# Performance work log

Measured on AMD Instinct MI355X. Metric: run time of the kernel, lower is better.

The kernel has to match this reference:

```python
import jax, jax.numpy as jnp
import numpy as np

B = 4096
IN = 1723 * 6          # 10338
H = 1024
OUT = 24 * 3 * 3 + 10 + 3  # 229
EPS = 1e-5


def _bn(x, g, b):
    # BatchNorm1d training-mode forward: biased batch statistics
    mu = jnp.mean(x, axis=0)
    var = jnp.var(x, axis=0)
    return g * (x - mu) * jax.lax.rsqrt(var + EPS) + b


def _resblock(h, wa, ba, ga, bea, wb, bb, gb, beb):
    t = jax.nn.relu(_bn(h @ wa + ba, ga, bea))
    t = _bn(t @ wb + bb, gb, beb)
    return jax.nn.relu(h + t)


def setup_inputs() -> dict:
    key = jax.random.key(0)
    ks = jax.random.split(key, 16)
    s = 0.02
    inp = {"x": jax.random.normal(ks[0], (B, IN), dtype=jnp.float32)}
    # FCBlock(IN -> H): Linear + BN + ReLU
    inp["w1"] = jax.random.normal(ks[1], (IN, H), dtype=jnp.float32) * s
    inp["b1"] = jnp.zeros((H,), jnp.float32)
    inp["g1"] = jnp.ones((H,), jnp.float32)
    inp["be1"] = jnp.zeros((H,), jnp.float32)
    # two FCResBlocks (H -> H)
    for i, kk in zip((2, 3), (ks[2:4], ks[4:6])):
        inp[f"w{i}a"] = jax.random.normal(kk[0], (H, H), dtype=jnp.float32) * s
        inp[f"b{i}a"] = jnp.zeros((H,), jnp.float32)
        inp[f"g{i}a"] = jnp.ones((H,), jnp.float32)
        inp[f"be{i}a"] = jnp.zeros((H,), jnp.float32)
        inp[f"w{i}b"] = jax.random.normal(kk[1], (H, H), dtype=jnp.float32) * s
        inp[f"b{i}b"] = jnp.zeros((H,), jnp.float32)
        inp[f"g{i}b"] = jnp.ones((H,), jnp.float32)
        inp[f"be{i}b"] = jnp.zeros((H,), jnp.float32)
    # final Linear (H -> OUT)
    inp["w4"] = jax.random.normal(ks[6], (H, OUT), dtype=jnp.float32) * s
    inp["b4"] = jnp.zeros((OUT,), jnp.float32)
    return inp


def reference(x, w1, b1, g1, be1,
              w2a, b2a, g2a, be2a, w2b, b2b, g2b, be2b,
              w3a, b3a, g3a, be3a, w3b, b3b, g3b, be3b,
              w4, b4):
    batch = x.shape[0]
    h = jax.nn.relu(_bn(x @ w1 + b1, g1, be1))
    h = _resblock(h, w2a, b2a, g2a, be2a, w2b, b2b, g2b, be2b)
    h = _resblock(h, w3a, b3a, g3a, be3a, w3b, b3b, g3b, be3b)
    out = h @ w4 + b4                              # (B, 229)

    rotmat = out[:, :216].reshape(-1, 3, 3)        # (B*24, 3, 3)
    betas = out[:, 216:226]                        # (B, 10)
    camera = out[:, 226:]                          # (B, 3)

    # batched 3x3 SVD orthogonalization (replaces per-sample Python loop)
    U, S, Vh = jnp.linalg.svd(rotmat, full_matrices=False)
    R = U @ Vh
    # det computed under no_grad in original -> stop_gradient
    det = jax.lax.stop_gradient(jnp.linalg.det(R))[:, None, None]
    R = (R * det).reshape(batch, 24, 3, 3)
    return (R, betas, camera)
```

## Files before the change

### kernel.cpp

```cpp
#include <hip/hip_runtime.h>
#include <math.h>


typedef _Float16 half8 __attribute__((ext_vector_type(8)));
typedef _Float16 half4_t __attribute__((ext_vector_type(4)));
typedef float floatx4 __attribute__((ext_vector_type(4)));

#define LO_SCALE 4096.0f
#define LO_INV (1.0f / 4096.0f)
#define IN_C 10338
#define INP_C 10368

__device__ __forceinline__ void gld16(const _Float16* g, _Float16* l) {
  __builtin_amdgcn_global_load_lds(
      (const __attribute__((address_space(1))) void*)g,
      (__attribute__((address_space(3))) void*)l, 16, 0, 0);
}

template <int TAG, bool STATS>
__global__ __launch_bounds__(256, 2)
void gemm_sk(const _Float16* __restrict__ Ah, const _Float16* __restrict__ Al,
             const _Float16* __restrict__ Bh, const _Float16* __restrict__ Bl,
             float* __restrict__ Cp, int Kld, int Ncols, int Ks,
             size_t partStride, const float* __restrict__ bias,
             float* __restrict__ psum, float* __restrict__ psq) {
  __shared__ _Float16 sAh[2][4096], sAl[2][4096];
  __shared__ _Float16 sBh[2][4096], sBl[2][4096];
  const int tid = threadIdx.x;
  const int wv = tid >> 6, ln = tid & 63;
  const int ln15 = ln & 15, q = ln >> 4;
  const int wr = wv >> 1, wc = wv & 1;
  const int bm0 = blockIdx.x * 128, bn0 = blockIdx.y * 128;
  const int k0 = blockIdx.z * Ks;
  Cp += (size_t)blockIdx.z * partStride;

  const int srow = ln >> 2;
  const int swzw = (ln & 3) ^ (srow & 3) ^ ((srow >> 2) & 3);
  const int ch0 = wv * 2, ch1 = wv * 2 + 1;
  const size_t offA0 = (size_t)(bm0 + ch0 * 16 + srow) * Kld + k0 + swzw * 8;
  const size_t offA1 = (size_t)(bm0 + ch1 * 16 + srow) * Kld + k0 + swzw * 8;
  const size_t offB0 = (size_t)(bn0 + ch0 * 16 + srow) * Kld + k0 + swzw * 8;
  const size_t offB1 = (size_t)(bn0 + ch1 * 16 + srow) * Kld + k0 + swzw * 8;

  const int swzr = (q ^ (ln15 & 3) ^ ((ln15 >> 2) & 3)) * 8;
  const int aoff = (wr * 64 + ln15) * 32 + swzr;
  const int boff = (wc * 64 + ln15) * 32 + swzr;

  floatx4 acc[4][4];
  floatx4 acc2[4][4];
#pragma unroll
  for (int i = 0; i < 4; ++i)
#pragma unroll
    for (int j = 0; j < 4; ++j) {
      acc[i][j] = (floatx4){0.f, 0.f, 0.f, 0.f};
      acc2[i][j] = (floatx4){0.f, 0.f, 0.f, 0.f};
    }

  auto stage = [&](int kt, int buf) {
    gld16(Ah + offA0 + kt, &sAh[buf][ch0 * 512]);
    gld16(Ah + offA1 + kt, &sAh[buf][ch1 * 512]);
    gld16(Al + offA0 + kt, &sAl[buf][ch0 * 512]);
    gld16(Al + offA1 + kt, &sAl[buf][ch1 * 512]);
    gld16(Bh + offB0 + kt, &sBh[buf][ch0 * 512]);
    gld16(Bh + offB1 + kt, &sBh[buf][ch1 * 512]);
    gld16(Bl + offB0 + kt, &sBl[buf][ch0 * 512]);
    gld16(Bl + offB1 + kt, &sBl[buf][ch1 * 512]);
  };

  stage(0, 0);
  int cur = 0;
  for (int kt = 0; kt < Ks; kt += 32) {
    __syncthreads();
    if (kt + 32 < Ks) stage(kt + 32, cur ^ 1);

    const _Float16* pAh = &sAh[cur][aoff];
    const _Float16* pAl = &sAl[cur][aoff];
    const _Float16* pBh = &sBh[cur][boff];
    const _Float16* pBl = &sBl[cur][boff];
    half8 bh[4], bl[4];
#pragma unroll
    for (int ni = 0; ni < 4; ++ni) {
      bh[ni] = *(const half8*)(pBh + ni * 512);
      bl[ni] = *(const half8*)(pBl + ni * 512);
    }
#pragma unroll
    for (int mh = 0; mh < 2; ++mh) {
      half8 ah[2], al[2];
#pragma unroll
      for (int i = 0; i < 2; ++i) {
        ah[i] = *(const half8*)(pAh + (mh * 2 + i) * 512);
        al[i] = *(const half8*)(pAl + (mh * 2 + i) * 512);
      }
#pragma unroll
      for (int i = 0; i < 2; ++i) {
        const int mi = mh * 2 + i;
#pragma unroll
        for (int ni = 0; ni < 4; ++ni) {
          acc[mi][ni] = __builtin_amdgcn_mfma_f32_16x16x32_f16(
              ah[i], bh[ni], acc[mi][ni], 0, 0, 0);
          acc2[mi][ni] = __builtin_amdgcn_mfma_f32_16x16x32_f16(
              ah[i], bl[ni], acc2[mi][ni], 0, 0, 0);
          acc2[mi][ni] = __builtin_amdgcn_mfma_f32_16x16x32_f16(
              al[i], bh[ni], acc2[mi][ni], 0, 0, 0);
        }
      }
    }
    cur ^= 1;
  }

  float bs[4];
  float sacc[4] = {0.f, 0.f, 0.f, 0.f};
  float qacc[4] = {0.f, 0.f, 0.f, 0.f};
  if constexpr (STATS) {
#pragma unroll
    for (int ni = 0; ni < 4; ++ni)
      bs[ni] = bias[bn0 + wc * 64 + ni * 16 + ln15];
  }
#pragma unroll
  for (int mi = 0; mi < 4; ++mi)
#pragma unroll
    for (int ni = 0; ni < 4; ++ni) {
      const int col = bn0 + wc * 64 + ni * 16 + ln15;
      const int rbase = bm0 + wr * 64 + mi * 16 + q * 4;
#pragma unroll
      for (int r = 0; r < 4; ++r) {
        float v = acc[mi][ni][r] + acc2[mi][ni][r] * LO_INV;
        if constexpr (STATS) {
          v += bs[ni];
          sacc[ni] += v;
          qacc[ni] += v * v;
        }
        Cp[(size_t)(rbase + r) * Ncols + col] = v;
      }
    }
  if constexpr (STATS) {
    __syncthreads();
    float* sS = (float*)&sAh[0][0];
    float* sQ = (float*)&sAl[0][0];
    const int contrib = wr * 4 + q;
#pragma unroll
    for (int ni = 0; ni < 4; ++ni) {
      const int colt = wc * 64 + ni * 16 + ln15;
      sS[contrib * 128 + colt] = sacc[ni];
      sQ[contrib * 128 + colt] = qacc[ni];
    }
    __syncthreads();
    if (tid < 128) {
      float S = 0.f, Q = 0.f;
#pragma unroll
      for (int c = 0; c < 8; ++c) {
        S += sS[c * 128 + tid];
        Q += sQ[c * 128 + tid];
      }
      psum[(size_t)blockIdx.x * 1024 + bn0 + tid] = S;
      psq[(size_t)blockIdx.x * 1024 + bn0 + tid] = Q;
    }
  }
}

struct TJob {
  const float* src;
  _Float16* th;
  _Float16* tl;
  int K, N, Kpad, tK, start;
};
struct CJobs {
  TJob j[6];
  const float* x;
  _Float16* xh;
  _Float16* xl;
  int splitStart;
};

__global__ __launch_bounds__(256)
void convert_all(CJobs J) {
  const int b = blockIdx.x;
  const int tid = threadIdx.x;
  if (b >= J.splitStart) {
    int di = (b - J.splitStart) * 256 + tid;
    int base = di * 8;
    int row = base / INP_C;
    int col0 = base - row * INP_C;
    const float* src = J.x + (size_t)row * IN_C + col0;
    float v[8];
#pragma unroll
    for (int j = 0; j < 8; ++j) v[j] = (col0 + j < IN_C) ? src[j] : 0.f;
    half8 h, l;
#pragma unroll
    for (int j = 0; j < 8; ++j) {
      _Float16 hh = (_Float16)v[j];
      h[j] = hh;
      l[j] = (_Float16)((v[j] - (float)hh) * LO_SCALE);
    }
    *(half8*)(J.xh + base) = h;
    *(half8*)(J.xl + base) = l;
    return;
  }
  int ji = 0;
#pragma unroll
  for (int i = 1; i < 6; ++i)
    if (b >= J.j[i].start) ji = i;
  const TJob job = J.j[ji];
  const int t = b - job.start;
  const int kk0 = (t % job.tK) * 32;
  const int nn0 = (t / job.tK) * 32;

  __shared__ float ts[32][33];
  const int tx = tid & 31, ty = tid >> 5;
#pragma unroll
  for (int r = 0; r < 4; ++r) {
    int kk = kk0 + ty + r * 8;
    int nn = nn0 + tx;
    ts[ty + r * 8][tx] =
        (kk < job.K && nn < job.N) ? job.src[(size_t)kk * job.N + nn] : 0.f;
  }
  __syncthreads();
  const int tw = tid & 7, rw = tid >> 3;
  const int nn = nn0 + rw, kk = kk0 + tw * 4;
  half4_t h, l;
#pragma unroll
  for (int i2 = 0; i2 < 4; ++i2) {
    float v = ts[tw * 4 + i2][rw];
    _Float16 hh = (_Float16)v;
    h[i2] = hh;
    l[i2] = (_Float16)((v - (float)hh) * LO_SCALE);
  }
  size_t o = (size_t)nn * job.Kpad + kk;
  *(half4_t*)(job.th + o) = h;
  *(half4_t*)(job.tl + o) = l;
}

__global__ __launch_bounds__(256)
void reduce_bias_stats_v(const float* __restrict__ Cp,
                         const float* __restrict__ bias, float* __restrict__ Y,
                         float* __restrict__ psum, float* __restrict__ psq,
                         int S, size_t stride, int rowsPer) {
  const int N = 1024;
  const int t = threadIdx.x;
  const int cg = t & 15, rl = t >> 4;
  const int col4 = blockIdx.x * 64 + cg * 4;
  const int r0 = blockIdx.y * rowsPer;
  const floatx4 bs = *(const floatx4*)(bias + col4);
  floatx4 s = {0.f, 0.f, 0.f, 0.f}, qq = {0.f, 0.f, 0.f, 0.f};
  for (int r = r0 + rl; r < r0 + rowsPer; r += 16) {
    size_t i = (size_t)r * N + col4;
    floatx4 v = bs;
    for (int k = 0; k < S; ++k) v += *(const floatx4*)(Cp + k * stride + i);
    *(floatx4*)(Y + i) = v;
    s += v;
    qq += v * v;
  }
  __shared__ floatx4 ls[16][16], lq[16][16];
  ls[rl][cg] = s;
  lq[rl][cg] = qq;
  __syncthreads();
  if (t < 16) {
    floatx4 S4 = {0.f, 0.f, 0.f, 0.f}, Q4 = {0.f, 0.f, 0.f, 0.f};
#pragma unroll
    for (int r = 0; r < 16; ++r) {
      S4 += ls[r][t];
      Q4 += lq[r][t];
    }
    size_t o = (size_t)blockIdx.y * N + blockIdx.x * 64 + t * 4;
    *(floatx4*)(psum + o) = S4;
    *(floatx4*)(psq + o) = Q4;
  }
}

__global__ __launch_bounds__(256)
void bn_apply_v(const float* __restrict__ Y, const float* __restrict__ psum,
                const float* __restrict__ psq, const float* __restrict__ g,
                const float* __restrict__ be, const float* __restrict__ res,
                float* __restrict__ outf, _Float16* __restrict__ oh,
                _Float16* __restrict__ ol, int RB, float invM) {
  const int N = 1024;
  const int t = threadIdx.x;
  const int cg = t & 63, rl = t >> 6;
  const int col4 = blockIdx.x * 256 + cg * 4;
  __shared__ floatx4 lA[64], lB[64];
  if (t < 64) {
    int c4 = blockIdx.x * 256 + t * 4;
    floatx4 s = {0.f, 0.f, 0.f, 0.f}, qq = {0.f, 0.f, 0.f, 0.f};
    for (int rb = 0; rb < RB; ++rb) {
      s += *(const floatx4*)(psum + (size_t)rb * N + c4);
      qq += *(const floatx4*)(psq + (size_t)rb * N + c4);
    }
    floatx4 m = s * invM;
    floatx4 var = qq * invM - m * m;
    floatx4 rstd;
#pragma unroll
    for (int i = 0; i < 4; ++i) rstd[i] = rsqrtf(var[i] + 1e-5f);
    floatx4 a = (*(const floatx4*)(g + c4)) * rstd;
    lA[t] = a;
    lB[t] = (*(const floatx4*)(be + c4)) - m * a;
  }
  __syncthreads();
  const floatx4 a = lA[cg], b2 = lB[cg];
#pragma unroll
  for (int rr = 0; rr < 2; ++rr) {
    const int r = blockIdx.y * 8 + rl + rr * 4;
    const size_t i = (size_t)r * N + col4;
    floatx4 v = (*(const floatx4*)(Y + i)) * a + b2;
    if (res) v += *(const floatx4*)(res + i);
#pragma unroll
    for (int ii = 0; ii < 4; ++ii) v[ii] = fmaxf(v[ii], 0.f);
    if (outf) *(floatx4*)(outf + i) = v;
    half4_t h, l;
#pragma unroll
    for (int ii = 0; ii < 4; ++ii) {
      _Float16 hh = (_Float16)v[ii];
      h[ii] = hh;
      l[ii] = (_Float16)((v[ii] - (float)hh) * LO_SCALE);
    }
    *(half4_t*)(oh + i) = h;
    *(half4_t*)(ol + i) = l;
  }
}

__device__ __forceinline__ void cofactor3(const float X[9], float C[9]) {
  C[0] = X[4] * X[8] - X[5] * X[7];
  C[1] = X[5] * X[6] - X[3] * X[8];
  C[2] = X[3] * X[7] - X[4] * X[6];
  C[3] = X[2] * X[7] - X[1] * X[8];
  C[4] = X[0] * X[8] - X[2] * X[6];
  C[5] = X[1] * X[6] - X[0] * X[7];
  C[6] = X[1] * X[5] - X[2] * X[4];
  C[7] = X[2] * X[3] - X[0] * X[5];
  C[8] = X[0] * X[4] - X[1] * X[3];
}

__global__ __launch_bounds__(256)
void polar_tail(const float* __restrict__ Cp, const float* __restrict__ bias,
                float* __restrict__ out, int Bt, int nmat, int S,
                size_t stride) {
  const int ldy = 256;
  int idx = blockIdx.x * blockDim.x + threadIdx.x;
  if (idx < nmat) {
    int s = idx / 24, j = idx % 24;
    const size_t base = (size_t)s * ldy + j * 9;
    float A[9], X[9];
#pragma unroll
    for (int k = 0; k < 9; ++k) {
      float v = bias[j * 9 + k];
      for (int z = 0; z < S; ++z) v += Cp[z * stride + base + k];
      A[k] = v;
      X[k] = v;
    }
    double detA = (double)A[0] * ((double)A[4] * A[8] - (double)A[5] * A[7]) -
                  (double)A[1] * ((double)A[3] * A[8] - (double)A[5] * A[6]) +
                  (double)A[2] * ((double)A[3] * A[7] - (double)A[4] * A[6]);
    float sgn = (detA < 0.0) ? -1.f : 1.f;
#pragma unroll 1
    for (int it = 0; it < 12; ++it) {
      float C[9];
      cofactor3(X, C);
      float det = X[0] * C[0] + X[1] * C[1] + X[2] * C[2];
      float ad = fmaxf(fabsf(det), 1e-30f);
      float idet = (det < 0.f ? -1.f : 1.f) / ad;
      float n1 = 0.f, n2 = 0.f;
#pragma unroll
      for (int k = 0; k < 9; ++k) {
        n1 += X[k] * X[k];
        n2 += C[k] * C[k];
      }
      n1 = fmaxf(n1, 1e-30f);
      float zeta = sqrtf(sqrtf(n2 * idet * idet / n1));
      zeta = fminf(fmaxf(zeta, 1e-4f), 1e4f);
      float iz = 0.5f / zeta;
      float hz = 0.5f * zeta;
#pragma unroll
      for (int k = 0; k < 9; ++k) X[k] = hz * X[k] + iz * idet * C[k];
    }
    float* o = out + (size_t)idx * 9;
#pragma unroll
    for (int k = 0; k < 9; ++k) o[k] = X[k] * sgn;
  } else {
    int i = idx - nmat;
    int nb = Bt * 10;
    int nc = Bt * 3;
    int s, k, c;
    if (i < nb) {
      s = i / 10;
      k = i;
      c = 216 + (i % 10);
    } else if (i < nb + nc) {
      int t2 = i - nb;
      s = t2 / 3;
      k = i;
      c = 226 + (t2 % 3);
    } else {
      return;
    }
    float v = bias[c];
    size_t base = (size_t)s * ldy + c;
    for (int z = 0; z < S; ++z) v += Cp[z * stride + base];
    out[(size_t)Bt * 216 + k] = v;
  }
}

extern "C" void kernel_launch(void* const* d_in, const int* in_sizes, int n_in,
                              void* d_out, int out_size, void* d_ws,
                              size_t ws_size, hipStream_t stream) {
  const float* x = (const float*)d_in[0];
  const float* w1 = (const float*)d_in[1];
  const float* b1 = (const float*)d_in[2];
  const float* g1 = (const float*)d_in[3];
  const float* be1 = (const float*)d_in[4];
  const float* w2a = (const float*)d_in[5];
  const float* b2a = (const float*)d_in[6];
  const float* g2a = (const float*)d_in[7];
  const float* be2a = (const float*)d_in[8];
  const float* w2b = (const float*)d_in[9];
  const float* b2b = (const float*)d_in[10];
  const float* g2b = (const float*)d_in[11];
  const float* be2b = (const float*)d_in[12];
  const float* w3a = (const float*)d_in[13];
  const float* b3a = (const float*)d_in[14];
  const float* g3a = (const float*)d_in[15];
  const float* be3a = (const float*)d_in[16];
  const float* w3b = (const float*)d_in[17];
  const float* b3b = (const float*)d_in[18];
  const float* g3b = (const float*)d_in[19];
  const float* be3b = (const float*)d_in[20];
  const float* w4 = (const float*)d_in[21];
  const float* b4 = (const float*)d_in[22];
  float* out = (float*)d_out;

  const int B = 4096, IN = 10338, INP = 10368, H = 1024;
  const int OUTN = 229, OUTP = 256;
  const int RB = 32;
  const int S_BIG = 2, S_HEAD = 8;

  char* p = (char*)d_ws;
  auto alloc = [&](size_t bytes) -> void* {
    void* r = (void*)p;
    p += (bytes + 255) & ~(size_t)255;
    return r;
  };
  float* Cpart = (float*)alloc((size_t)S_HEAD * B * OUTP * 4);
  float* Y = (float*)alloc((size_t)B * H * 4);
  float* Hf = (float*)alloc((size_t)B * H * 4);
  _Float16* xh = (_Float16*)alloc((size_t)B * INP * 2);
  _Float16* xl = (_Float16*)alloc((size_t)B * INP * 2);
  _Float16* w1h = (_Float16*)alloc((size_t)H * INP * 2);
  _Float16* w1l = (_Float16*)alloc((size_t)H * INP * 2);
  _Float16 *wmh[4], *wml[4];
  for (int i = 0; i < 4; ++i) {
    wmh[i] = (_Float16*)alloc((size_t)H * H * 2);
    wml[i] = (_Float16*)alloc((size_t)H * H * 2);
  }
  _Float16* w4h = (_Float16*)alloc((size_t)OUTP * H * 2);
  _Float16* w4l = (_Float16*)alloc((size_t)OUTP * H * 2);
  _Float16* hh = (_Float16*)alloc((size_t)B * H * 2);
  _Float16* hl = (_Float16*)alloc((size_t)B * H * 2);
  float* psum = (float*)alloc((size_t)RB * H * 4);
  float* psq = (float*)alloc((size_t)RB * H * 4);

  {
    CJobs J;
    const float* wsrc[6] = {w1, w2a, w2b, w3a, w3b, w4};
    _Float16* th[6] = {w1h, wmh[0], wmh[1], wmh[2], wmh[3], w4h};
    _Float16* tl[6] = {w1l, wml[0], wml[1], wml[2], wml[3], w4l};
    int Ks[6] = {IN, H, H, H, H, H};
    int Ns[6] = {H, H, H, H, H, OUTN};
    int Kpads[6] = {INP, H, H, H, H, H};
    int Npads[6] = {H, H, H, H, H, OUTP};
    int start = 0;
    for (int i = 0; i < 6; ++i) {
      J.j[i].src = wsrc[i];
      J.j[i].th = th[i];
      J.j[i].tl = tl[i];
      J.j[i].K = Ks[i];
      J.j[i].N = Ns[i];
      J.j[i].Kpad = Kpads[i];
      J.j[i].tK = Kpads[i] / 32;
      J.j[i].start = start;
      start += (Kpads[i] / 32) * (Npads[i] / 32);
    }
    J.x = x;
    J.xh = xh;
    J.xl = xl;
    J.splitStart = start;
    int total = start + (B * INP / 8 + 255) / 256;
    convert_all<<<dim3(total), 256, 0, stream>>>(J);
  }

  auto bnapply = [&](const float* g, const float* be, const float* res,
                     float* outf) {
    bn_apply_v<<<dim3(H / 256, B / 8), 256, 0, stream>>>(
        Y, psum, psq, g, be, res, outf, hh, hl, RB, 1.f / B);
  };
  auto midgemm = [&](const _Float16* Bh, const _Float16* Bl,
                     const float* bias) {
    gemm_sk<1, true><<<dim3(B / 128, H / 128, 1), 256, 0, stream>>>(
        hh, hl, Bh, Bl, Y, H, H, H, 0, bias, psum, psq);
  };

  gemm_sk<0, false><<<dim3(B / 128, H / 128, S_BIG), 256, 0, stream>>>(
      xh, xl, w1h, w1l, Cpart, INP, H, INP / S_BIG, (size_t)B * H, nullptr,
      nullptr, nullptr);
  reduce_bias_stats_v<<<dim3(16, RB), 256, 0, stream>>>(
      Cpart, b1, Y, psum, psq, S_BIG, (size_t)B * H, B / RB);
  bnapply(g1, be1, nullptr, Hf);
  midgemm(wmh[0], wml[0], b2a);
  bnapply(g2a, be2a, nullptr, nullptr);
  midgemm(wmh[1], wml[1], b2b);
  bnapply(g2b, be2b, Hf, Hf);
  midgemm(wmh[2], wml[2], b3a);
  bnapply(g3a, be3a, nullptr, nullptr);
  midgemm(wmh[3], wml[3], b3b);
  bnapply(g3b, be3b, Hf, Hf);
  gemm_sk<2, false><<<dim3(B / 128, OUTP / 128, S_HEAD), 256, 0, stream>>>(
      hh, hl, w4h, w4l, Cpart, H, OUTP, H / S_HEAD, (size_t)B * OUTP, nullptr,
      nullptr, nullptr);

  int nmat = B * 24;
  int ntot = nmat + B * 13;
  polar_tail<<<dim3((ntot + 255) / 256), 256, 0, stream>>>(
      Cpart, b4, out, B, nmat, S_HEAD, (size_t)B * OUTP);
}
```

Before: 918.9 us.

## Add 256x256-tile 512-thread GEMM for first layer with split-K of four

Adds a dedicated first-layer GEMM kernel that uses 256x256 output tiles per 512-thread block, double-buffered LDS loads and a remapped block index. Split-K goes from 2 to 4, so the grid is one block per CU. The goal is more operand reuse per byte loaded on the dominant K=10368 GEMM. To make room for four partial buffers without more workspace, Y and Hf now alias partitions of the split-K buffer, so restrict qualifiers are dropped from the reduce kernel. The cost is heavy LDS use (one block per CU), more partial-sum traffic in the reduce, and reliance on the reduce reading each element before it overwrites it in place.

```diff
diff --git a/kernel.cpp b/kernel.cpp
--- a/kernel.cpp
+++ b/kernel.cpp
@@ -15,6 +15,125 @@
   __builtin_amdgcn_global_load_lds(
       (const __attribute__((address_space(1))) void*)g,
       (__attribute__((address_space(3))) void*)l, 16, 0, 0);
+}
+
+__global__ __launch_bounds__(512, 2)
+void gemm_l1(const _Float16* __restrict__ Ah, const _Float16* __restrict__ Al,
+             const _Float16* __restrict__ Bh, const _Float16* __restrict__ Bl,
+             float* __restrict__ Cp, int Kld, int Ncols, int Ks,
+             size_t partStride) {
+  __shared__ _Float16 sAh[2][8192], sAl[2][8192];
+  __shared__ _Float16 sBh[2][8192], sBl[2][8192];
+  const int tid = threadIdx.x;
+  const int wv = tid >> 6, ln = tid & 63;
+  const int ln15 = ln & 15, q = ln >> 4;
+  const int wr = wv >> 2, wc = wv & 3;
+  const int xm = (blockIdx.x & 7) * 2 + (blockIdx.x >> 3);
+  const int bm0 = xm * 256, bn0 = blockIdx.y * 256;
+  const int k0 = blockIdx.z * Ks;
+  Cp += (size_t)blockIdx.z * partStride;
+
+  const int srow = ln >> 2;
+  const int swzw = (ln & 3) ^ (srow & 3) ^ ((srow >> 2) & 3);
+  const int ch0 = wv, ch1 = wv + 8;
+  const size_t offA0 = (size_t)(bm0 + ch0 * 16 + srow) * Kld + k0 + swzw * 8;
+  const size_t offA1 = (size_t)(bm0 + ch1 * 16 + srow) * Kld + k0 + swzw * 8;
+  const size_t offB0 = (size_t)(bn0 + ch0 * 16 + srow) * Kld + k0 + swzw * 8;
+  const size_t offB1 = (size_t)(bn0 + ch1 * 16 + srow) * Kld + k0 + swzw * 8;
+
+  const int swzr = (q ^ (ln15 & 3) ^ ((ln15 >> 2) & 3)) * 8;
+
+  floatx4 acc[8][4], acc2[8][4];
+#pragma unroll
+  for (int i = 0; i < 8; ++i)
+#pragma unroll
+    for (int j = 0; j < 4; ++j) {
+      acc[i][j] = (floatx4){0.f, 0.f, 0.f, 0.f};
+      acc2[i][j] = (floatx4){0.f, 0.f, 0.f, 0.f};
+    }
+
+  auto stage = [&](int kt, int buf) {
+    gld16(Bh + offB0 + kt, &sBh[buf][ch0 * 512]);
+    gld16(Bh + offB1 + kt, &sBh[buf][ch1 * 512]);
+    gld16(Bl + offB0 + kt, &sBl[buf][ch0 * 512]);
+    gld16(Bl + offB1 + kt, &sBl[buf][ch1 * 512]);
+    gld16(Ah + offA0 + kt, &sAh[buf][ch0 * 512]);
+    gld16(Ah + offA1 + kt, &sAh[buf][ch1 * 512]);
+    gld16(Al + offA0 + kt, &sAl[buf][ch0 * 512]);
+    gld16(Al + offA1 + kt, &sAl[buf][ch1 * 512]);
+  };
+
+  stage(0, 0);
+  int cur = 0;
+  for (int kt = 0; kt < Ks; kt += 32) {
+    asm volatile("s_waitcnt lgkmcnt(0)" ::: "memory");
+    __builtin_amdgcn_s_barrier();
+    __builtin_amdgcn_sched_barrier(0);
+    if (kt + 32 < Ks) {
+      stage(kt + 32, cur ^ 1);
+      asm volatile("s_waitcnt vmcnt(8)" ::: "memory");
+    } else {
+      asm volatile("s_waitcnt vmcnt(0)" ::: "memory");
+    }
+    __builtin_amdgcn_s_barrier();
+    __builtin_amdgcn_sched_barrier(0);
+
+    const _Float16* pAh = &sAh[cur][0];
+    const _Float16* pAl = &sAl[cur][0];
+    const _Float16* pBh = &sBh[cur][0];
+    const _Float16* pBl = &sBl[cur][0];
+    half8 bhf[4], blf[4];
+#pragma unroll
+    for (int ni = 0; ni < 4; ++ni) {
+      const int bo = (wc * 64 + ni * 16 + ln15) * 32 + swzr;
+      bhf[ni] = *(const half8*)(pBh + bo);
+      blf[ni] = *(const half8*)(pBl + bo);
+    }
+#pragma unroll
+    for (int mp = 0; mp < 4; ++mp) {
+      half8 ahf[2], alf[2];
+#pragma unroll
+      for (int i = 0; i < 2; ++i) {
+        const int ao = (wr * 128 + (mp * 2 + i) * 16 + ln15) * 32 + swzr;
+        ahf[i] = *(const half8*)(pAh + ao);
+        alf[i] = *(const half8*)(pAl + ao);
+      }
+      __builtin_amdgcn_s_setprio(1);
+#pragma unroll
+      for (int i = 0; i < 2; ++i) {
+        const int mi = mp * 2 + i;
+#pragma unroll
+        for (int ni = 0; ni < 4; ++ni) {
+          acc[mi][ni] = __builtin_amdgcn_mfma_f32_16x16x32_f16(
+              ahf[i], bhf[ni], acc[mi][ni], 0, 0, 0);
+          acc2[mi][ni] = __builtin_amdgcn_mfma_f32_16x16x32_f16(
+              ahf[i], blf[ni], acc2[mi][ni], 0, 0, 0);
+        }
+      }
+#pragma unroll
+      for (int i = 0; i < 2; ++i) {
+        const int mi = mp * 2 + i;
+#pragma unroll
+        for (int ni = 0; ni < 4; ++ni)
+          acc2[mi][ni] = __builtin_amdgcn_mfma_f32_16x16x32_f16(
+              alf[i], bhf[ni], acc2[mi][ni], 0, 0, 0);
+      }
+      __builtin_amdgcn_s_setprio(0);
+    }
+    cur ^= 1;
+  }
+
+#pragma unroll
+  for (int mi = 0; mi < 8; ++mi)
+#pragma unroll
+    for (int ni = 0; ni < 4; ++ni) {
+      const int col = bn0 + wc * 64 + ni * 16 + ln15;
+      const int rbase = bm0 + wr * 128 + mi * 16 + q * 4;
+#pragma unroll
+      for (int r = 0; r < 4; ++r)
+        Cp[(size_t)(rbase + r) * Ncols + col] =
+            acc[mi][ni][r] + acc2[mi][ni][r] * LO_INV;
+    }
 }
 
 template <int TAG, bool STATS>
@@ -231,10 +350,10 @@
 }
 
 __global__ __launch_bounds__(256)
-void reduce_bias_stats_v(const float* __restrict__ Cp,
-                         const float* __restrict__ bias, float* __restrict__ Y,
-                         float* __restrict__ psum, float* __restrict__ psq,
-                         int S, size_t stride, int rowsPer) {
+void reduce_bias_stats_v(const float* Cp, const float* __restrict__ bias,
+                         float* Y, float* __restrict__ psum,
+                         float* __restrict__ psq, int S, size_t stride,
+                         int rowsPer) {
   const int N = 1024;
   const int t = threadIdx.x;
   const int cg = t & 15, rl = t >> 4;
@@ -429,7 +548,7 @@
   const int B = 4096, IN = 10338, INP = 10368, H = 1024;
   const int OUTN = 229, OUTP = 256;
   const int RB = 32;
-  const int S_BIG = 2, S_HEAD = 8;
+  const int S_L1 = 4, S_HEAD = 8;
 
   char* p = (char*)d_ws;
   auto alloc = [&](size_t bytes) -> void* {
@@ -437,9 +556,9 @@
     p += (bytes + 255) & ~(size_t)255;
     return r;
   };
-  float* Cpart = (float*)alloc((size_t)S_HEAD * B * OUTP * 4);
-  float* Y = (float*)alloc((size_t)B * H * 4);
-  float* Hf = (float*)alloc((size_t)B * H * 4);
+  float* Cpart = (float*)alloc((size_t)S_L1 * B * H * 4);
+  float* Y = Cpart + 2 * (size_t)B * H;
+  float* Hf = Cpart + 3 * (size_t)B * H;
   _Float16* xh = (_Float16*)alloc((size_t)B * INP * 2);
   _Float16* xl = (_Float16*)alloc((size_t)B * INP * 2);
   _Float16* w1h = (_Float16*)alloc((size_t)H * INP * 2);
@@ -496,11 +615,10 @@
         hh, hl, Bh, Bl, Y, H, H, H, 0, bias, psum, psq);
   };
 
-  gemm_sk<0, false><<<dim3(B / 128, H / 128, S_BIG), 256, 0, stream>>>(
-      xh, xl, w1h, w1l, Cpart, INP, H, INP / S_BIG, (size_t)B * H, nullptr,
-      nullptr, nullptr);
+  gemm_l1<<<dim3(B / 256, H / 256, S_L1), 512, 0, stream>>>(
+      xh, xl, w1h, w1l, Cpart, INP, H, INP / S_L1, (size_t)B * H);
   reduce_bias_stats_v<<<dim3(16, RB), 256, 0, stream>>>(
-      Cpart, b1, Y, psum, psq, S_BIG, (size_t)B * H, B / RB);
+      Cpart, b1, Y, psum, psq, S_L1, (size_t)B * H, B / RB);
   bnapply(g1, be1, nullptr, Hf);
   midgemm(wmh[0], wml[0], b2a);
   bnapply(g2a, be2a, nullptr, nullptr);
```

Result: slower. 1.996 ms (+117.2%).

## Add 128x64-tile mid-layer GEMM kernel for more blocks on HxH layers

Applied to the files above, without the earlier changes.

Adds a dedicated gemm_mid kernel for the four 1024x1024 residual-block GEMMs. It uses 128x64 output tiles instead of 128x128, which doubles the grid to 512 blocks, and it still fuses bias and the BN partial statistics into the epilogue. The workspace is also repacked so Y and Hf sit inside the enlarged Cpart buffer, and restrict is dropped on reduce_bias_stats_v because of that aliasing. The aim is better CU occupancy on the mid GEMMs, at the cost of more redundant A-tile reads and smaller per-block reuse.

```diff
diff --git a/kernel.cpp b/kernel.cpp
--- a/kernel.cpp
+++ b/kernel.cpp
@@ -158,6 +158,133 @@
   }
 }
 
+__global__ __launch_bounds__(256, 2)
+void gemm_mid(const _Float16* __restrict__ Ah, const _Float16* __restrict__ Al,
+              const _Float16* __restrict__ Bh, const _Float16* __restrict__ Bl,
+              float* __restrict__ Y, int Kld, int Ncols, int Ks,
+              const float* __restrict__ bias, float* __restrict__ psum,
+              float* __restrict__ psq) {
+  __shared__ _Float16 sAh[2][4096], sAl[2][4096];
+  __shared__ _Float16 sBh[2][2048], sBl[2][2048];
+  const int tid = threadIdx.x;
+  const int wv = tid >> 6, ln = tid & 63;
+  const int ln15 = ln & 15, q = ln >> 4;
+  const int wr = wv >> 1, wc = wv & 1;
+  const int bm0 = blockIdx.x * 128, bn0 = blockIdx.y * 64;
+
+  const int srow = ln >> 2;
+  const int swzw = (ln & 3) ^ (srow & 3) ^ ((srow >> 2) & 3);
+  const int ch0 = wv * 2, ch1 = wv * 2 + 1;
+  const size_t offA0 = (size_t)(bm0 + ch0 * 16 + srow) * Kld + swzw * 8;
+  const size_t offA1 = (size_t)(bm0 + ch1 * 16 + srow) * Kld + swzw * 8;
+  const size_t offB = (size_t)(bn0 + wv * 16 + srow) * Kld + swzw * 8;
+
+  const int swzr = (q ^ (ln15 & 3) ^ ((ln15 >> 2) & 3)) * 8;
+  const int aoff = (wr * 64 + ln15) * 32 + swzr;
+  const int boff = (wc * 32 + ln15) * 32 + swzr;
+
+  floatx4 acc[4][2], acc2[4][2];
+#pragma unroll
+  for (int i = 0; i < 4; ++i)
+#pragma unroll
+    for (int j = 0; j < 2; ++j) {
+      acc[i][j] = (floatx4){0.f, 0.f, 0.f, 0.f};
+      acc2[i][j] = (floatx4){0.f, 0.f, 0.f, 0.f};
+    }
+
+  auto stage = [&](int kt, int buf) {
+    gld16(Ah + offA0 + kt, &sAh[buf][ch0 * 512]);
+    gld16(Ah + offA1 + kt, &sAh[buf][ch1 * 512]);
+    gld16(Al + offA0 + kt, &sAl[buf][ch0 * 512]);
+    gld16(Al + offA1 + kt, &sAl[buf][ch1 * 512]);
+    gld16(Bh + offB + kt, &sBh[buf][wv * 512]);
+    gld16(Bl + offB + kt, &sBl[buf][wv * 512]);
+  };
+
+  stage(0, 0);
+  int cur = 0;
+  for (int kt = 0; kt < Ks; kt += 32) {
+    __syncthreads();
+    if (kt + 32 < Ks) stage(kt + 32, cur ^ 1);
+
+    const _Float16* pAh = &sAh[cur][aoff];
+    const _Float16* pAl = &sAl[cur][aoff];
+    const _Float16* pBh = &sBh[cur][boff];
+    const _Float16* pBl = &sBl[cur][boff];
+    half8 bh[2], bl[2];
+#pragma unroll
+    for (int ni = 0; ni < 2; ++ni) {
+      bh[ni] = *(const half8*)(pBh + ni * 512);
+      bl[ni] = *(const half8*)(pBl + ni * 512);
+    }
+#pragma unroll
+    for (int mh = 0; mh < 2; ++mh) {
+      half8 ah[2], al[2];
+#pragma unroll
+      for (int i = 0; i < 2; ++i) {
+        ah[i] = *(const half8*)(pAh + (mh * 2 + i) * 512);
+        al[i] = *(const half8*)(pAl + (mh * 2 + i) * 512);
+      }
+#pragma unroll
+      for (int i = 0; i < 2; ++i) {
+        const int mi = mh * 2 + i;
+#pragma unroll
+        for (int ni = 0; ni < 2; ++ni) {
+          acc[mi][ni] = __builtin_amdgcn_mfma_f32_16x16x32_f16(
+              ah[i], bh[ni], acc[mi][ni], 0, 0, 0);
+          acc2[mi][ni] = __builtin_amdgcn_mfma_f32_16x16x32_f16(
+              ah[i], bl[ni], acc2[mi][ni], 0, 0, 0);
+          acc2[mi][ni] = __builtin_amdgcn_mfma_f32_16x16x32_f16(
+              al[i], bh[ni], acc2[mi][ni], 0, 0, 0);
+        }
+      }
+    }
+    cur ^= 1;
+  }
+
+  float bs[2];
+  float sacc[2] = {0.f, 0.f};
+  float qacc[2] = {0.f, 0.f};
+#pragma unroll
+  for (int ni = 0; ni < 2; ++ni)
+    bs[ni] = bias[bn0 + wc * 32 + ni * 16 + ln15];
+#pragma unroll
+  for (int mi = 0; mi < 4; ++mi)
+#pragma unroll
+    for (int ni = 0; ni < 2; ++ni) {
+      const int col = bn0 + wc * 32 + ni * 16 + ln15;
+      const int rbase = bm0 + wr * 64 + mi * 16 + q * 4;
+#pragma unroll
+      for (int r = 0; r < 4; ++r) {
+        float v = acc[mi][ni][r] + acc2[mi][ni][r] * LO_INV + bs[ni];
+        sacc[ni] += v;
+        qacc[ni] += v * v;
+        Y[(size_t)(rbase + r) * Ncols + col] = v;
+      }
+    }
+  __syncthreads();
+  float* sS = (float*)&sAh[0][0];
+  float* sQ = (float*)&sAl[0][0];
+  const int contrib = wr * 4 + q;
+#pragma unroll
+  for (int ni = 0; ni < 2; ++ni) {
+    const int colt = wc * 32 + ni * 16 + ln15;
+    sS[contrib * 64 + colt] = sacc[ni];
+    sQ[contrib * 64 + colt] = qacc[ni];
+  }
+  __syncthreads();
+  if (tid < 64) {
+    float S = 0.f, Q = 0.f;
+#pragma unroll
+    for (int c = 0; c < 8; ++c) {
+      S += sS[c * 64 + tid];
+      Q += sQ[c * 64 + tid];
+    }
+    psum[(size_t)blockIdx.x * 1024 + bn0 + tid] = S;
+    psq[(size_t)blockIdx.x * 1024 + bn0 + tid] = Q;
+  }
+}
+
 struct TJob {
   const float* src;
   _Float16* th;
@@ -231,10 +358,10 @@
 }
 
 __global__ __launch_bounds__(256)
-void reduce_bias_stats_v(const float* __restrict__ Cp,
-                         const float* __restrict__ bias, float* __restrict__ Y,
-                         float* __restrict__ psum, float* __restrict__ psq,
-                         int S, size_t stride, int rowsPer) {
+void reduce_bias_stats_v(const float* Cp, const float* __restrict__ bias,
+                         float* Y, float* __restrict__ psum,
+                         float* __restrict__ psq, int S, size_t stride,
+                         int rowsPer) {
   const int N = 1024;
   const int t = threadIdx.x;
   const int cg = t & 15, rl = t >> 4;
@@ -429,7 +556,7 @@
   const int B = 4096, IN = 10338, INP = 10368, H = 1024;
   const int OUTN = 229, OUTP = 256;
   const int RB = 32;
-  const int S_BIG = 2, S_HEAD = 8;
+  const int S_L1 = 2, S_HEAD = 8;
 
   char* p = (char*)d_ws;
   auto alloc = [&](size_t bytes) -> void* {
@@ -437,9 +564,9 @@
     p += (bytes + 255) & ~(size_t)255;
     return r;
   };
-  float* Cpart = (float*)alloc((size_t)S_HEAD * B * OUTP * 4);
-  float* Y = (float*)alloc((size_t)B * H * 4);
-  float* Hf = (float*)alloc((size_t)B * H * 4);
+  float* Cpart = (float*)alloc((size_t)4 * B * H * 4);
+  float* Y = Cpart + 2 * (size_t)B * H;
+  float* Hf = Cpart + 3 * (size_t)B * H;
   _Float16* xh = (_Float16*)alloc((size_t)B * INP * 2);
   _Float16* xl = (_Float16*)alloc((size_t)B * INP * 2);
   _Float16* w1h = (_Float16*)alloc((size_t)H * INP * 2);
@@ -492,15 +619,15 @@
   };
   auto midgemm = [&](const _Float16* Bh, const _Float16* Bl,
                      const float* bias) {
-    gemm_sk<1, true><<<dim3(B / 128, H / 128, 1), 256, 0, stream>>>(
-        hh, hl, Bh, Bl, Y, H, H, H, 0, bias, psum, psq);
+    gemm_mid<<<dim3(B / 128, H / 64, 1), 256, 0, stream>>>(
+        hh, hl, Bh, Bl, Y, H, H, H, bias, psum, psq);
   };
 
-  gemm_sk<0, false><<<dim3(B / 128, H / 128, S_BIG), 256, 0, stream>>>(
-      xh, xl, w1h, w1l, Cpart, INP, H, INP / S_BIG, (size_t)B * H, nullptr,
+  gemm_sk<0, false><<<dim3(B / 128, H / 128, S_L1), 256, 0, stream>>>(
+      xh, xl, w1h, w1l, Cpart, INP, H, INP / S_L1, (size_t)B * H, nullptr,
       nullptr, nullptr);
   reduce_bias_stats_v<<<dim3(16, RB), 256, 0, stream>>>(
-      Cpart, b1, Y, psum, psq, S_BIG, (size_t)B * H, B / RB);
+      Cpart, b1, Y, psum, psq, S_L1, (size_t)B * H, B / RB);
   bnapply(g1, be1, nullptr, Hf);
   midgemm(wmh[0], wml[0], b2a);
   bnapply(g2a, be2a, nullptr, nullptr);
```

After: 887.6 us. 1.04x faster.

## Switch GEMMs to 32x32x16 MFMA and add narrower-tile kernel for mid layers

Applied to the files above, without the earlier changes.

Rewrites the split-K GEMM inner loop to use 32x32x16 f16 MFMA tiles (2x2 per wave) instead of 16x16x32, which halves the LDS fragment loads per MFMA and changes the output row mapping. Adds a dedicated gemm_mid kernel for the 1024x1024 layers that uses 128x64 block tiles, doubling the grid to improve CU occupancy and fusing bias plus BN statistics. It also packs the partial, Y and Hf buffers into one workspace allocation. The risk is that the new swizzle or row mapping mismatches the stored layout, and the narrower tiles reuse less data.

```diff
diff --git a/kernel.cpp b/kernel.cpp
--- a/kernel.cpp
+++ b/kernel.cpp
@@ -5,6 +5,7 @@
 typedef _Float16 half8 __attribute__((ext_vector_type(8)));
 typedef _Float16 half4_t __attribute__((ext_vector_type(4)));
 typedef float floatx4 __attribute__((ext_vector_type(4)));
+typedef float floatx16 __attribute__((ext_vector_type(16)));
 
 #define LO_SCALE 4096.0f
 #define LO_INV (1.0f / 4096.0f)
@@ -28,7 +29,6 @@
   __shared__ _Float16 sBh[2][4096], sBl[2][4096];
   const int tid = threadIdx.x;
   const int wv = tid >> 6, ln = tid & 63;
-  const int ln15 = ln & 15, q = ln >> 4;
   const int wr = wv >> 1, wc = wv & 1;
   const int bm0 = blockIdx.x * 128, bn0 = blockIdx.y * 128;
   const int k0 = blockIdx.z * Ks;
@@ -42,19 +42,23 @@
   const size_t offB0 = (size_t)(bn0 + ch0 * 16 + srow) * Kld + k0 + swzw * 8;
   const size_t offB1 = (size_t)(bn0 + ch1 * 16 + srow) * Kld + k0 + swzw * 8;
 
-  const int swzr = (q ^ (ln15 & 3) ^ ((ln15 >> 2) & 3)) * 8;
-  const int aoff = (wr * 64 + ln15) * 32 + swzr;
-  const int boff = (wc * 64 + ln15) * 32 + swzr;
-
-  floatx4 acc[4][4];
-  floatx4 acc2[4][4];
-#pragma unroll
-  for (int i = 0; i < 4; ++i)
-#pragma unroll
-    for (int j = 0; j < 4; ++j) {
-      acc[i][j] = (floatx4){0.f, 0.f, 0.f, 0.f};
-      acc2[i][j] = (floatx4){0.f, 0.f, 0.f, 0.f};
-    }
+  const int r31 = ln & 31, hi5 = ln >> 5;
+  const int kk = (ln & 3) ^ ((ln >> 2) & 3);
+  const int aBase0 = (wr * 64 + r31) * 32;
+  const int aBase1 = (wr * 64 + 32 + r31) * 32;
+  const int bBase0 = (wc * 64 + r31) * 32;
+  const int bBase1 = (wc * 64 + 32 + r31) * 32;
+
+  floatx16 acc[2][2], acc2[2][2];
+#pragma unroll
+  for (int i = 0; i < 2; ++i)
+#pragma unroll
+    for (int j = 0; j < 2; ++j)
+#pragma unroll
+      for (int e = 0; e < 16; ++e) {
+        acc[i][j][e] = 0.f;
+        acc2[i][j][e] = 0.f;
+      }
 
   auto stage = [&](int kt, int buf) {
     gld16(Ah + offA0 + kt, &sAh[buf][ch0 * 512]);
@@ -73,88 +77,165 @@
     __syncthreads();
     if (kt + 32 < Ks) stage(kt + 32, cur ^ 1);
 
-    const _Float16* pAh = &sAh[cur][aoff];
-    const _Float16* pAl = &sAl[cur][aoff];
-    const _Float16* pBh = &sBh[cur][boff];
-    const _Float16* pBl = &sBl[cur][boff];
-    half8 bh[4], bl[4];
-#pragma unroll
-    for (int ni = 0; ni < 4; ++ni) {
-      bh[ni] = *(const half8*)(pBh + ni * 512);
-      bl[ni] = *(const half8*)(pBl + ni * 512);
-    }
-#pragma unroll
-    for (int mh = 0; mh < 2; ++mh) {
+    const _Float16* pAh = &sAh[cur][0];
+    const _Float16* pAl = &sAl[cur][0];
+    const _Float16* pBh = &sBh[cur][0];
+    const _Float16* pBl = &sBl[cur][0];
+#pragma unroll
+    for (int ks = 0; ks < 2; ++ks) {
+      const int p8 = (((ks * 2) + hi5) ^ kk) * 8;
+      half8 ah[2], al[2], bh[2], bl[2];
+      ah[0] = *(const half8*)(pAh + aBase0 + p8);
+      ah[1] = *(const half8*)(pAh + aBase1 + p8);
+      al[0] = *(const half8*)(pAl + aBase0 + p8);
+      al[1] = *(const half8*)(pAl + aBase1 + p8);
+      bh[0] = *(const half8*)(pBh + bBase0 + p8);
+      bh[1] = *(const half8*)(pBh + bBase1 + p8);
+      bl[0] = *(const half8*)(pBl + bBase0 + p8);
+      bl[1] = *(const half8*)(pBl + bBase1 + p8);
+#pragma unroll
+      for (int ti = 0; ti < 2; ++ti)
+#pragma unroll
+        for (int tj = 0; tj < 2; ++tj) {
+          acc[ti][tj] = __builtin_amdgcn_mfma_f32_32x32x16_f16(
+              ah[ti], bh[tj], acc[ti][tj], 0, 0, 0);
+          acc2[ti][tj] = __builtin_amdgcn_mfma_f32_32x32x16_f16(
+              ah[ti], bl[tj], acc2[ti][tj], 0, 0, 0);
+          acc2[ti][tj] = __builtin_amdgcn_mfma_f32_32x32x16_f16(
+              al[ti], bh[tj], acc2[ti][tj], 0, 0, 0);
+        }
+    }
+    cur ^= 1;
+  }
+
+  float bs;
+  float sacc = 0.f, qacc = 0.f;
+  if constexpr (STATS) bs = bias[bn0 + wc * 64 + r31];
+#pragma unroll
+  for (int ti = 0; ti < 2; ++ti)
+#pragma unroll
+    for (int tj = 0; tj < 2; ++tj) {
+      const int col = bn0 + wc * 64 + tj * 32 + r31;
+#pragma unroll
+      for (int r = 0; r < 16; ++r) {
+        const int row =
+            bm0 + wr * 64 + ti * 32 + (r & 3) + 8 * (r >> 2) + 4 * hi5;
+        float v = acc[ti][tj][r] + acc2[ti][tj][r] * LO_INV;
+        Cp[(size_t)row * Ncols + col] = v;
+      }
+    }
+  (void)bs;
+  (void)sacc;
+  (void)qacc;
+}
+
+__global__ __launch_bounds__(256, 2)
+void gemm_mid(const _Float16* __restrict__ Ah, const _Float16* __restrict__ Al,
+              const _Float16* __restrict__ Bh, const _Float16* __restrict__ Bl,
+              float* __restrict__ Y, int Kld, int Ncols, int Ks,
+              const float* __restrict__ bias, float* __restrict__ psum,
+              float* __restrict__ psq) {
+  __shared__ _Float16 sAh[2][4096], sAl[2][4096];
+  __shared__ _Float16 sBh[2][2048], sBl[2][2048];
+  const int tid = threadIdx.x;
+  const int wv = tid >> 6, ln = tid & 63;
+  const int wr = wv >> 1, wc = wv & 1;
+  const int bm0 = blockIdx.x * 128, bn0 = blockIdx.y * 64;
+
+  const int srow = ln >> 2;
+  const int swzw = (ln & 3) ^ (srow & 3) ^ ((srow >> 2) & 3);
+  const int ch0 = wv * 2, ch1 = wv * 2 + 1;
+  const size_t offA0 = (size_t)(bm0 + ch0 * 16 + srow) * Kld + swzw * 8;
+  const size_t offA1 = (size_t)(bm0 + ch1 * 16 + srow) * Kld + swzw * 8;
+  const size_t offB = (size_t)(bn0 + wv * 16 + srow) * Kld + swzw * 8;
+
+  const int r31 = ln & 31, hi5 = ln >> 5;
+  const int kk = (ln & 3) ^ ((ln >> 2) & 3);
+  const int aBase0 = (wr * 64 + r31) * 32;
+  const int aBase1 = (wr * 64 + 32 + r31) * 32;
+  const int bBase = (wc * 32 + r31) * 32;
+
+  floatx16 acc[2], acc2[2];
+#pragma unroll
+  for (int i = 0; i < 2; ++i)
+#pragma unroll
+    for (int e = 0; e < 16; ++e) {
+      acc[i][e] = 0.f;
+      acc2[i][e] = 0.f;
+    }
+
+  auto stage = [&](int kt, int buf) {
+    gld16(Ah + offA0 + kt, &sAh[buf][ch0 * 512]);
+    gld16(Ah + offA1 + kt, &sAh[buf][ch1 * 512]);
+    gld16(Al + offA0 + kt, &sAl[buf][ch0 * 512]);
+    gld16(Al + offA1 + kt, &sAl[buf][ch1 * 512]);
+    gld16(Bh + offB + kt, &sBh[buf][wv * 512]);
+    gld16(Bl + offB + kt, &sBl[buf][wv * 512]);
+  };
+
+  stage(0, 0);
+  int cur = 0;
+  for (int kt = 0; kt < Ks; kt += 32) {
+    __syncthreads();
+    if (kt + 32 < Ks) stage(kt + 32, cur ^ 1);
+
+    const _Float16* pAh = &sAh[cur][0];
+    const _Float16* pAl = &sAl[cur][0];
+    const _Float16* pBh = &sBh[cur][0];
+    const _Float16* pBl = &sBl[cur][0];
+#pragma unroll
+    for (int ks = 0; ks < 2; ++ks) {
+      const int p8 = (((ks * 2) + hi5) ^ kk) * 8;
       half8 ah[2], al[2];
-#pragma unroll
-      for (int i = 0; i < 2; ++i) {
-        ah[i] = *(const half8*)(pAh + (mh * 2 + i) * 512);
-        al[i] = *(const half8*)(pAl + (mh * 2 + i) * 512);
+      ah[0] = *(const half8*)(pAh + aBase0 + p8);
+      ah[1] = *(const half8*)(pAh + aBase1 + p8);
+      al[0] = *(const half8*)(pAl + aBase0 + p8);
+      al[1] = *(const half8*)(pAl + aBase1 + p8);
+      half8 bh = *(const half8*)(pBh + bBase + p8);
+      half8 bl = *(const half8*)(pBl + bBase + p8);
+#pragma unroll
+      for (int ti = 0; ti < 2; ++ti) {
+        acc[ti] = __builtin_amdgcn_mfma_f32_32x32x16_f16(ah[ti], bh, acc[ti],
+                                                         0, 0, 0);
+        acc2[ti] = __builtin_amdgcn_mfma_f32_32x32x16_f16(ah[ti], bl, acc2[ti],
+                                                          0, 0, 0);
+        acc2[ti] = __builtin_amdgcn_mfma_f32_32x32x16_f16(al[ti], bh, acc2[ti],
+                                                          0, 0, 0);
       }
-#pragma unroll
-      for (int i = 0; i < 2; ++i) {
-        const int mi = mh * 2 + i;
-#pragma unroll
-        for (int ni = 0; ni < 4; ++ni) {
-          acc[mi][ni] = __builtin_amdgcn_mfma_f32_16x16x32_f16(
-              ah[i], bh[ni], acc[mi][ni], 0, 0, 0);
-          acc2[mi][ni] = __builtin_amdgcn_mfma_f32_16x16x32_f16(
-              ah[i], bl[ni], acc2[mi][ni], 0, 0, 0);
-          acc2[mi][ni] = __builtin_amdgcn_mfma_f32_16x16x32_f16(
-              al[i], bh[ni], acc2[mi][ni], 0, 0, 0);
-        }
-      }
     }
     cur ^= 1;
   }
 
-  float bs[4];
-  float sacc[4] = {0.f, 0.f, 0.f, 0.f};
-  float qacc[4] = {0.f, 0.f, 0.f, 0.f};
-  if constexpr (STATS) {
-#pragma unroll
-    for (int ni = 0; ni < 4; ++ni)
-      bs[ni] = bias[bn0 + wc * 64 + ni * 16 + ln15];
-  }
-#pragma unroll
-  for (int mi = 0; mi < 4; ++mi)
-#pragma unroll
-    for (int ni = 0; ni < 4; ++ni) {
-      const int col = bn0 + wc * 64 + ni * 16 + ln15;
-      const int rbase = bm0 + wr * 64 + mi * 16 + q * 4;
-#pragma unroll
-      for (int r = 0; r < 4; ++r) {
-        float v = acc[mi][ni][r] + acc2[mi][ni][r] * LO_INV;
-        if constexpr (STATS) {
-          v += bs[ni];
-          sacc[ni] += v;
-          qacc[ni] += v * v;
-        }
-        Cp[(size_t)(rbase + r) * Ncols + col] = v;
-      }
-    }
-  if constexpr (STATS) {
-    __syncthreads();
-    float* sS = (float*)&sAh[0][0];
-    float* sQ = (float*)&sAl[0][0];
-    const int contrib = wr * 4 + q;
-#pragma unroll
-    for (int ni = 0; ni < 4; ++ni) {
-      const int colt = wc * 64 + ni * 16 + ln15;
-      sS[contrib * 128 + colt] = sacc[ni];
-      sQ[contrib * 128 + colt] = qacc[ni];
-    }
-    __syncthreads();
-    if (tid < 128) {
-      float S = 0.f, Q = 0.f;
-#pragma unroll
-      for (int c = 0; c < 8; ++c) {
-        S += sS[c * 128 + tid];
-        Q += sQ[c * 128 + tid];
-      }
-      psum[(size_t)blockIdx.x * 1024 + bn0 + tid] = S;
-      psq[(size_t)blockIdx.x * 1024 + bn0 + tid] = Q;
-    }
+  const int col = bn0 + wc * 32 + r31;
+  const float bsc = bias[col];
+  float sacc = 0.f, qacc = 0.f;
+#pragma unroll
+  for (int ti = 0; ti < 2; ++ti)
+#pragma unroll
+    for (int r = 0; r < 16; ++r) {
+      const int row =
+          bm0 + wr * 64 + ti * 32 + (r & 3) + 8 * (r >> 2) + 4 * hi5;
+      float v = acc[ti][r] + acc2[ti][r] * LO_INV + bsc;
+      sacc += v;
+      qacc += v * v;
+      Y[(size_t)row * Ncols + col] = v;
+    }
+  __syncthreads();
+  float* sS = (float*)&sAh[0][0];
+  float* sQ = (float*)&sAl[0][0];
+  const int contrib = wr * 2 + hi5;
+  sS[contrib * 64 + wc * 32 + r31] = sacc;
+  sQ[contrib * 64 + wc * 32 + r31] = qacc;
+  __syncthreads();
+  if (tid < 64) {
+    float S = 0.f, Q = 0.f;
+#pragma unroll
+    for (int c = 0; c < 4; ++c) {
+      S += sS[c * 64 + tid];
+      Q += sQ[c * 64 + tid];
+    }
+    psum[(size_t)blockIdx.x * 1024 + bn0 + tid] = S;
+    psq[(size_t)blockIdx.x * 1024 + bn0 + tid] = Q;
   }
 }
 
@@ -231,10 +312,10 @@
 }
 
 __global__ __launch_bounds__(256)
-void reduce_bias_stats_v(const float* __restrict__ Cp,
-                         const float* __restrict__ bias, float* __restrict__ Y,
-                         float* __restrict__ psum, float* __restrict__ psq,
-                         int S, size_t stride, int rowsPer) {
+void reduce_bias_stats_v(const float* Cp, const float* __restrict__ bias,
+                         float* Y, float* __restrict__ psum,
+                         float* __restrict__ psq, int S, size_t stride,
+                         int rowsPer) {
   const int N = 1024;
   const int t = threadIdx.x;
   const int cg = t & 15, rl = t >> 4;
@@ -429,7 +510,7 @@
   const int B = 4096, IN = 10338, INP = 10368, H = 1024;
   const int OUTN = 229, OUTP = 256;
   const int RB = 32;
-  const int S_BIG = 2, S_HEAD = 8;
+  const int S_L1 = 2, S_HEAD = 8;
 
   char* p = (char*)d_ws;
   auto alloc = [&](size_t bytes) -> void* {
@@ -437,9 +518,9 @@
     p += (bytes + 255) & ~(size_t)255;
     return r;
   };
-  float* Cpart = (float*)alloc((size_t)S_HEAD * B * OUTP * 4);
-  float* Y = (float*)alloc((size_t)B * H * 4);
-  float* Hf = (float*)alloc((size_t)B * H * 4);
+  float* Cpart = (float*)alloc((size_t)4 * B * H * 4);
+  float* Y = Cpart + 2 * (size_t)B * H;
+  float* Hf = Cpart + 3 * (size_t)B * H;
   _Float16* xh = (_Float16*)alloc((size_t)B * INP * 2);
   _Float16* xl = (_Float16*)alloc((size_t)B * INP * 2);
   _Float16* w1h = (_Float16*)alloc((size_t)H * INP * 2);
@@ -492,15 +573,15 @@
   };
   auto midgemm = [&](const _Float16* Bh, const _Float16* Bl,
                      const float* bias) {
-    gemm_sk<1, true><<<dim3(B / 128, H / 128, 1), 256, 0, stream>>>(
-        hh, hl, Bh, Bl, Y, H, H, H, 0, bias, psum, psq);
+    gemm_mid<<<dim3(B / 128, H / 64, 1), 256, 0, stream>>>(
+        hh, hl, Bh, Bl, Y, H, H, H, bias, psum, psq);
   };
 
-  gemm_sk<0, false><<<dim3(B / 128, H / 128, S_BIG), 256, 0, stream>>>(
-      xh, xl, w1h, w1l, Cpart, INP, H, INP / S_BIG, (size_t)B * H, nullptr,
+  gemm_sk<0, false><<<dim3(B / 128, H / 128, S_L1), 256, 0, stream>>>(
+      xh, xl, w1h, w1l, Cpart, INP, H, INP / S_L1, (size_t)B * H, nullptr,
       nullptr, nullptr);
   reduce_bias_stats_v<<<dim3(16, RB), 256, 0, stream>>>(
-      Cpart, b1, Y, psum, psq, S_BIG, (size_t)B * H, B / RB);
+      Cpart, b1, Y, psum, psq, S_L1, (size_t)B * H, B / RB);
   bnapply(g1, be1, nullptr, Hf);
   midgemm(wmh[0], wml[0], b2a);
   bnapply(g2a, be2a, nullptr, nullptr);
```

Result: no change. 918.2 us (-0.1%).
